# Kernel tuning notes

Measured on AMD Instinct MI355X. Metric: run time of the kernel, lower is better.

Reference implementation:

```python
import jax, jax.numpy as jnp
import numpy as np

N = 8192
D_MODEL = 256
D_K = 128
NUM_MOL = 512  # molecule_index values in [0, NUM_MOL); output rows = max(idx)+1, fixed here for jit


def setup_inputs() -> dict:
    key = jax.random.key(0)
    k1, k2, k3, k4, k5, k6, k7, k8 = jax.random.split(key, 8)
    fragments = jax.random.normal(k1, (N, D_MODEL), dtype=jnp.float32)
    molecule_index = jnp.sort(jax.random.randint(k2, (N,), 0, NUM_MOL, dtype=jnp.int64))
    s = 1.0 / np.sqrt(D_MODEL)
    Wq = jax.random.uniform(k3, (D_MODEL, D_K), jnp.float32, -s, s)
    bq = jax.random.uniform(k4, (D_K,), jnp.float32, -s, s)
    Wk = jax.random.uniform(k5, (D_MODEL, D_K), jnp.float32, -s, s)
    bk = jax.random.uniform(k6, (D_K,), jnp.float32, -s, s)
    Wv = jax.random.uniform(k7, (D_MODEL, D_K), jnp.float32, -s, s)
    bv = jax.random.uniform(k8, (D_K,), jnp.float32, -s, s)
    return {"fragments": fragments, "molecule_index": molecule_index,
            "Wq": Wq, "bq": bq, "Wk": Wk, "bk": bk, "Wv": Wv, "bv": bv}


def reference(fragments, molecule_index, Wq, bq, Wk, bk, Wv, bv):
    scale = jnp.asarray(np.sqrt(D_K), fragments.dtype)
    Q = fragments @ Wq + bq  # [N, d_k]
    K = fragments @ Wk + bk
    V = fragments @ Wv + bv
    scores = (Q / scale) @ K.T  # [N, N]
    same_mol = molecule_index[:, None] == molecule_index[None, :]
    scores = jnp.where(same_mol, scores, -jnp.inf)
    weights = jax.nn.softmax(scores, axis=-1)  # block-diagonal rows
    out = weights @ V  # [N, d_k]
    # scatter_add per-molecule pooling
    mol_emb = jax.ops.segment_sum(out, molecule_index, num_segments=NUM_MOL)
    return mol_emb
```

## Files before the change

### kernel.cpp

```cpp
#include <hip/hip_runtime.h>
#include <hip/hip_bf16.h>

#define D_MODEL 256
#define D_K 128
#define CH 48

typedef short bf16x8 __attribute__((ext_vector_type(8)));
typedef float f32x4 __attribute__((ext_vector_type(4)));

__device__ inline unsigned short f2bf(float x) {
    union { float f; unsigned u; } v; v.f = x;
    unsigned r = v.u + 0x7FFFu + ((v.u >> 16) & 1u);
    return (unsigned short)(r >> 16);
}
__device__ inline float bf2f(unsigned short h) {
    union { unsigned u; float f; } v; v.u = ((unsigned)h) << 16; return v.f;
}

#define AT_BYTE(r, c2) (((r) << 9) + ((((c2) << 1)) ^ (((r) & 7) << 4)))

__device__ __forceinline__ int wave_lb(const int* __restrict__ p, int stride, int n, int val, int guess) {
    const int lane = threadIdx.x & 63;
    int base = guess - 32;
    while (true) {
        int idx = base + lane;
        int v;
        if (idx < 0)        v = -2147483647 - 1;
        else if (idx >= n)  v = 2147483647;
        else                v = p[(size_t)idx * stride];
        unsigned long long ge = __ballot(v >= val);
        if (ge == 0ULL) { base += 64; continue; }
        int v0 = __shfl(v, 0);
        if (v0 >= val && base > 0) { base -= 63; continue; }
        return base + (__ffsll((unsigned long long)ge) - 1);
    }
}

__device__ __forceinline__ bf16x8 w_frag(const float* __restrict__ W, int cc, int k0, int g) {
    const float* p = W + (size_t)(k0 + g * 8) * D_K + cc;
    unsigned short t8[8];
    #pragma unroll
    for (int j = 0; j < 8; ++j) t8[j] = f2bf(p[(size_t)j * D_K]);
    return *(const bf16x8*)t8;
}

template<int NRT>
__device__ __forceinline__ void qkv_tiles(
    const unsigned char* lds,
    const float* __restrict__ Wq, const float* __restrict__ Wk, const float* __restrict__ Wv,
    int wave, int lr, int g, f32x4 (&acc)[6][NRT])
{
    #pragma unroll
    for (int cl = 0; cl < 6; ++cl) {
        const int ct = wave + cl * 4;
        const int which = ct >> 3, cc = (ct & 7) * 16 + lr;
        const float* W = which == 0 ? Wq : (which == 1 ? Wk : Wv);
        #pragma unroll
        for (int k0 = 0; k0 < 8; ++k0) {
            bf16x8 bf = w_frag(W, cc, k0 * 32, g);
            #pragma unroll
            for (int rt = 0; rt < NRT; ++rt) {
                bf16x8 af = *(const bf16x8*)(lds + AT_BYTE(rt * 16 + lr, k0 * 32 + g * 8));
                acc[cl][rt] = __builtin_amdgcn_mfma_f32_16x16x32_bf16(af, bf, acc[cl][rt], 0, 0, 0);
            }
        }
    }
}

template<int NRT>
__device__ __forceinline__ void fast_path(
    const float* __restrict__ A,
    const float* __restrict__ Wq, const float* __restrict__ bq,
    const float* __restrict__ Wk, const float* __restrict__ bk,
    const float* __restrict__ Wv, const float* __restrict__ bv,
    float* __restrict__ out, unsigned char* lds, int s, int m, int mol)
{
    unsigned short* Qb = (unsigned short*)(lds + 24576);
    unsigned short* Kb = (unsigned short*)(lds + 37632);
    unsigned short* Vb = (unsigned short*)(lds);
    unsigned short* S  = (unsigned short*)(lds + 50688);
    float* rinv = (float*)(lds + 55680);
    float* csum = (float*)(lds + 55872);
    float* emb  = (float*)(lds + 56064);

    const int tid = threadIdx.x;
    const int wave = tid >> 6, lane = tid & 63;
    const int lr = lane & 15, g = lane >> 4;

    #pragma unroll
    for (int it = 0; it < NRT * 4; ++it) {
        int eidx = tid * 4 + it * 1024;
        int r = eidx >> 8, c = eidx & 255;
        float4 a;
        if (r < m) a = *(const float4*)&A[(size_t)(s + r) * D_MODEL + c];
        else       a = make_float4(0.f, 0.f, 0.f, 0.f);
        unsigned short o[4] = {f2bf(a.x), f2bf(a.y), f2bf(a.z), f2bf(a.w)};
        *(unsigned long long*)(lds + AT_BYTE(r, c)) = *(const unsigned long long*)o;
    }
    __syncthreads();

    f32x4 acc[6][NRT];
    #pragma unroll
    for (int i = 0; i < 6; ++i)
        #pragma unroll
        for (int j = 0; j < NRT; ++j) acc[i][j] = {0.f, 0.f, 0.f, 0.f};
    qkv_tiles<NRT>(lds, Wq, Wk, Wv, wave, lr, g, acc);
    __syncthreads();

    const float qs = 0.08838834764831845f;
    #pragma unroll
    for (int cl = 0; cl < 6; ++cl) {
        int ct = wave + cl * 4;
        int which = ct >> 3;
        int col = (ct & 7) * 16 + lr;
        const float* bsrc = which == 0 ? bq : (which == 1 ? bk : bv);
        float bb = bsrc[col];
        float sc = which == 0 ? qs : 1.f;
        unsigned short* dst = which == 0 ? Qb : (which == 1 ? Kb : Vb);
        #pragma unroll
        for (int rt = 0; rt < NRT; ++rt) {
            int rbase = rt * 16 + g * 4;
            #pragma unroll
            for (int r = 0; r < 4; ++r)
                dst[(rbase + r) * 136 + col] = f2bf((acc[cl][rt][r] + bb) * sc);
        }
    }
    __syncthreads();

    for (int job = wave; job < NRT * NRT; job += 4) {
        int ti = job / NRT, tj = job % NRT;
        f32x4 sa = {0.f, 0.f, 0.f, 0.f};
        #pragma unroll
        for (int kk = 0; kk < 4; ++kk) {
            bf16x8 qf = *(const bf16x8*)&Qb[(ti * 16 + lr) * 136 + kk * 32 + g * 8];
            bf16x8 kf = *(const bf16x8*)&Kb[(tj * 16 + lr) * 136 + kk * 32 + g * 8];
            sa = __builtin_amdgcn_mfma_f32_16x16x32_bf16(qf, kf, sa, 0, 0, 0);
        }
        int jcol = tj * 16 + lr, ibase = ti * 16 + g * 4;
        #pragma unroll
        for (int r = 0; r < 4; ++r)
            S[(ibase + r) * 52 + jcol] = f2bf(sa[r]);
    }
    __syncthreads();

    {
        int row = tid >> 2, sub = tid & 3;
        if (row < m) {
            float mx = -3.4e38f;
            for (int j = sub; j < m; j += 4) mx = fmaxf(mx, bf2f(S[row * 52 + j]));
            mx = fmaxf(mx, __shfl_xor(mx, 1));
            mx = fmaxf(mx, __shfl_xor(mx, 2));
            float sum = 0.f;
            for (int j = sub; j < m; j += 4) {
                float ev = __expf(bf2f(S[row * 52 + j]) - mx);
                S[row * 52 + j] = f2bf(ev);
                sum += ev;
            }
            sum += __shfl_xor(sum, 1);
            sum += __shfl_xor(sum, 2);
            if (sub == 0) rinv[row] = 1.f / sum;
        }
    }
    __syncthreads();

    {
        int col = tid >> 2, sub = tid & 3;
        if (col < m) {
            float a = 0.f;
            for (int i = sub; i < m; i += 4) a += bf2f(S[i * 52 + col]) * rinv[i];
            a += __shfl_xor(a, 1);
            a += __shfl_xor(a, 2);
            if (sub == 0) csum[col] = a;
        }
    }
    __syncthreads();

    {
        int d = tid & 127, h = tid >> 7;
        float a = 0.f;
        for (int j = h; j < m; j += 2) a += csum[j] * bf2f(Vb[j * 136 + d]);
        emb[h * D_K + d] = a;
        __syncthreads();
        if (tid < D_K) out[(size_t)mol * D_K + tid] = emb[tid] + emb[D_K + tid];
    }
}

__global__ __launch_bounds__(256, 2) void fused_one(
    const float* __restrict__ A,
    const float* __restrict__ Wq, const float* __restrict__ bq,
    const float* __restrict__ Wk, const float* __restrict__ bk,
    const float* __restrict__ Wv, const float* __restrict__ bv,
    const int* __restrict__ midx,
    float* __restrict__ out,
    float* __restrict__ Qw, float* __restrict__ Kw, float* __restrict__ Vw,
    float* __restrict__ ML, int n, int nmol)
{
    __shared__ __align__(16) unsigned char lds[57088];
    int* se = (int*)(lds + 55680);

    const int tid = threadIdx.x, mol = blockIdx.x;
    const int wave = tid >> 6;

    const int stride = (midx[n - 1] == 0) ? 2 : 1;

    if (wave == 0) {
        int s_ = wave_lb(midx, stride, n, mol, (int)(((long long)mol * n) / nmol));
        if ((tid & 63) == 0) se[0] = s_;
    } else if (wave == 1) {
        int e_ = wave_lb(midx, stride, n, mol + 1, (int)(((long long)(mol + 1) * n) / nmol));
        if ((tid & 63) == 0) se[1] = e_;
    }
    __syncthreads();
    const int s = se[0], e = se[1];
    const int m = e - s;
    __syncthreads();

    if (m == 0) {
        if (tid < D_K) out[(size_t)mol * D_K + tid] = 0.f;
        return;
    }
    if (m <= 16) { fast_path<1>(A, Wq, bq, Wk, bk, Wv, bv, out, lds, s, m, mol); return; }
    if (m <= 32) { fast_path<2>(A, Wq, bq, Wk, bk, Wv, bv, out, lds, s, m, mol); return; }
    if (m <= 48) { fast_path<3>(A, Wq, bq, Wk, bk, Wv, bv, out, lds, s, m, mol); return; }

    const int lane = tid & 63;
    const int lr = lane & 15, g = lane >> 4;
    const float qs = 0.08838834764831845f;
    float* emb = (float*)(lds + 56064);

    for (int r0 = 0; r0 < m; r0 += CH) {
        #pragma unroll
        for (int it = 0; it < (CH * 256) / 1024; ++it) {
            int eidx = tid * 4 + it * 1024;
            int r = eidx >> 8, c = eidx & 255;
            float4 a;
            if (r0 + r < m) a = *(const float4*)&A[(size_t)(s + r0 + r) * D_MODEL + c];
            else            a = make_float4(0.f, 0.f, 0.f, 0.f);
            unsigned short o[4] = {f2bf(a.x), f2bf(a.y), f2bf(a.z), f2bf(a.w)};
            *(unsigned long long*)(lds + AT_BYTE(r, c)) = *(const unsigned long long*)o;
        }
        __syncthreads();

        f32x4 acc[6][3];
        #pragma unroll
        for (int i = 0; i < 6; ++i)
            #pragma unroll
            for (int j = 0; j < 3; ++j) acc[i][j] = {0.f, 0.f, 0.f, 0.f};
        qkv_tiles<3>(lds, Wq, Wk, Wv, wave, lr, g, acc);

        #pragma unroll
        for (int cl = 0; cl < 6; ++cl) {
            int ct = wave + cl * 4;
            int which = ct >> 3;
            int col = (ct & 7) * 16 + lr;
            const float* bsrc = which == 0 ? bq : (which == 1 ? bk : bv);
            float bb = bsrc[col];
            float sc = which == 0 ? qs : 1.f;
            float* dst = which == 0 ? Qw : (which == 1 ? Kw : Vw);
            #pragma unroll
            for (int rt = 0; rt < 3; ++rt) {
                int rbase = rt * 16 + g * 4;
                #pragma unroll
                for (int r = 0; r < 4; ++r) {
                    int lrow = rbase + r;
                    if (r0 + lrow < m)
                        dst[(size_t)(s + r0 + lrow) * D_K + col] = (acc[cl][rt][r] + bb) * sc;
                }
            }
        }
        __syncthreads();
    }

    if (tid < D_K) emb[tid] = 0.f;
    float* Mv = ML;
    float* Lv = ML + n;
    __threadfence();
    __syncthreads();

    for (int i = tid; i < m; i += 256) {
        const float4* q = (const float4*)(Qw + (size_t)(s + i) * D_K);
        float mx = -3.4e38f, sum = 0.f;
        for (int j = 0; j < m; ++j) {
            const float4* k = (const float4*)(Kw + (size_t)(s + j) * D_K);
            float sc = 0.f;
            #pragma unroll
            for (int t = 0; t < D_K / 4; ++t) {
                float4 a = q[t], b = k[t];
                sc += a.x * b.x + a.y * b.y + a.z * b.z + a.w * b.w;
            }
            if (sc > mx) { sum = sum * __expf(mx - sc) + 1.f; mx = sc; }
            else         { sum += __expf(sc - mx); }
        }
        Mv[s + i] = mx;
        Lv[s + i] = 1.f / sum;
    }
    __threadfence();
    __syncthreads();

    for (int j = tid; j < m; j += 256) {
        const float4* k = (const float4*)(Kw + (size_t)(s + j) * D_K);
        float cj = 0.f;
        for (int i = 0; i < m; ++i) {
            const float4* q = (const float4*)(Qw + (size_t)(s + i) * D_K);
            float sc = 0.f;
            #pragma unroll
            for (int t = 0; t < D_K / 4; ++t) {
                float4 a = q[t], b = k[t];
                sc += a.x * b.x + a.y * b.y + a.z * b.z + a.w * b.w;
            }
            cj += __expf(sc - Mv[s + i]) * Lv[s + i];
        }
        const float* v = Vw + (size_t)(s + j) * D_K;
        for (int d = 0; d < D_K; ++d) atomicAdd(&emb[d], cj * v[d]);
    }
    __syncthreads();
    if (tid < D_K) out[(size_t)mol * D_K + tid] = emb[tid];
}

extern "C" void kernel_launch(void* const* d_in, const int* in_sizes, int n_in,
                              void* d_out, int out_size, void* d_ws, size_t ws_size,
                              hipStream_t stream) {
    const float* frag = (const float*)d_in[0];
    const int*   midx = (const int*)d_in[1];
    const float* Wq = (const float*)d_in[2];
    const float* bq = (const float*)d_in[3];
    const float* Wk = (const float*)d_in[4];
    const float* bk = (const float*)d_in[5];
    const float* Wv = (const float*)d_in[6];
    const float* bv = (const float*)d_in[7];
    float* out = (float*)d_out;

    const int n = in_sizes[1];
    const int nmol = out_size / D_K;

    float* Qw = (float*)d_ws;
    float* Kw = Qw + (size_t)n * D_K;
    float* Vw = Kw + (size_t)n * D_K;
    float* ML = Vw + (size_t)n * D_K;

    fused_one<<<nmol, 256, 0, stream>>>(frag, Wq, bq, Wk, bk, Wv, bv, midx,
                                        out, Qw, Kw, Vw, ML, n, nmol);
}
```

Baseline: 19.80 us.

## Process molecule pairs per 512-thread block with masked joint attention tile

Each block now handles two consecutive molecules with 512 threads, packing both into one tile of up to 64 rows and masking cross-molecule scores to a large negative value so one softmax pass covers both. Weight fragments are now loaded by 8 waves with 3 column tiles each instead of 4 waves with 6, and a 64-row fast path is added. The aim is to halve block count, spread the W loads over more waves and fill MFMA tiles better for small molecules (about 16 rows on average). In exchange it uses more LDS per block, occupancy drops to one block per CU, and the masked tile computes wasted cross-molecule scores.

Measured after the change: 17.20 us. 13.2% less time.

```diff
diff --git a/kernel.cpp b/kernel.cpp
--- a/kernel.cpp
+++ b/kernel.cpp
@@ -4,6 +4,7 @@
 #define D_MODEL 256
 #define D_K 128
 #define CH 48
+#define NEG_BF16 ((unsigned short)0xFF7F)
 
 typedef short bf16x8 __attribute__((ext_vector_type(8)));
 typedef float f32x4 __attribute__((ext_vector_type(4)));
@@ -18,6 +19,12 @@
 }
 
 #define AT_BYTE(r, c2) (((r) << 9) + ((((c2) << 1)) ^ (((r) & 7) << 4)))
+#define QB_OFF 32768
+#define KB_OFF 50176
+#define S_OFF  67584
+#define RINV_OFF 76288
+#define CSUM_OFF 76544
+#define EMB_OFF  76800
 
 __device__ __forceinline__ int wave_lb(const int* __restrict__ p, int stride, int n, int val, int guess) {
     const int lane = threadIdx.x & 63;
@@ -48,11 +55,11 @@
 __device__ __forceinline__ void qkv_tiles(
     const unsigned char* lds,
     const float* __restrict__ Wq, const float* __restrict__ Wk, const float* __restrict__ Wv,
-    int wave, int lr, int g, f32x4 (&acc)[6][NRT])
+    int wave, int lr, int g, f32x4 (&acc)[3][NRT])
 {
     #pragma unroll
-    for (int cl = 0; cl < 6; ++cl) {
-        const int ct = wave + cl * 4;
+    for (int cl = 0; cl < 3; ++cl) {
+        const int ct = wave + cl * 8;
         const int which = ct >> 3, cc = (ct & 7) * 16 + lr;
         const float* W = which == 0 ? Wq : (which == 1 ? Wk : Wv);
         #pragma unroll
@@ -68,124 +75,252 @@
 }
 
 template<int NRT>
-__device__ __forceinline__ void fast_path(
+__device__ __forceinline__ void fast_pair(
+    const float* __restrict__ A,
+    const float* __restrict__ Wq, const float* __restrict__ bq,
+    const float* __restrict__ Wk, const float* __restrict__ bk,
+    const float* __restrict__ Wv, const float* __restrict__ bv,
+    float* __restrict__ out, unsigned char* lds,
+    int s, int mtot, int c1, int mol0, int mol1, bool w0, bool w1)
+{
+    unsigned short* Qb = (unsigned short*)(lds + QB_OFF);
+    unsigned short* Kb = (unsigned short*)(lds + KB_OFF);
+    unsigned short* Vb = (unsigned short*)(lds);
+    unsigned short* S  = (unsigned short*)(lds + S_OFF);
+    float* rinv = (float*)(lds + RINV_OFF);
+    float* csum = (float*)(lds + CSUM_OFF);
+    float* emb  = (float*)(lds + EMB_OFF);
+
+    const int tid = threadIdx.x;
+    const int wave = tid >> 6, lane = tid & 63;
+    const int lr = lane & 15, g = lane >> 4;
+
+    #pragma unroll
+    for (int it = 0; it < NRT * 2; ++it) {
+        int eidx = tid * 4 + it * 2048;
+        int r = eidx >> 8, c = eidx & 255;
+        float4 a;
+        if (r < mtot) a = *(const float4*)&A[(size_t)(s + r) * D_MODEL + c];
+        else          a = make_float4(0.f, 0.f, 0.f, 0.f);
+        unsigned short o[4] = {f2bf(a.x), f2bf(a.y), f2bf(a.z), f2bf(a.w)};
+        *(unsigned long long*)(lds + AT_BYTE(r, c)) = *(const unsigned long long*)o;
+    }
+    __syncthreads();
+
+    f32x4 acc[3][NRT];
+    #pragma unroll
+    for (int i = 0; i < 3; ++i)
+        #pragma unroll
+        for (int j = 0; j < NRT; ++j) acc[i][j] = {0.f, 0.f, 0.f, 0.f};
+    qkv_tiles<NRT>(lds, Wq, Wk, Wv, wave, lr, g, acc);
+    __syncthreads();
+
+    const float qs = 0.08838834764831845f;
+    #pragma unroll
+    for (int cl = 0; cl < 3; ++cl) {
+        int ct = wave + cl * 8;
+        int which = ct >> 3;
+        int col = (ct & 7) * 16 + lr;
+        const float* bsrc = which == 0 ? bq : (which == 1 ? bk : bv);
+        float bb = bsrc[col];
+        float sc = which == 0 ? qs : 1.f;
+        unsigned short* dst = which == 0 ? Qb : (which == 1 ? Kb : Vb);
+        #pragma unroll
+        for (int rt = 0; rt < NRT; ++rt) {
+            int rbase = rt * 16 + g * 4;
+            #pragma unroll
+            for (int r = 0; r < 4; ++r)
+                dst[(rbase + r) * 136 + col] = f2bf((acc[cl][rt][r] + bb) * sc);
+        }
+    }
+    __syncthreads();
+
+    for (int job = wave; job < NRT * NRT; job += 8) {
+        int ti = job / NRT, tj = job % NRT;
+        f32x4 sa = {0.f, 0.f, 0.f, 0.f};
+        #pragma unroll
+        for (int kk = 0; kk < 4; ++kk) {
+            bf16x8 qf = *(const bf16x8*)&Qb[(ti * 16 + lr) * 136 + kk * 32 + g * 8];
+            bf16x8 kf = *(const bf16x8*)&Kb[(tj * 16 + lr) * 136 + kk * 32 + g * 8];
+            sa = __builtin_amdgcn_mfma_f32_16x16x32_bf16(qf, kf, sa, 0, 0, 0);
+        }
+        int jcol = tj * 16 + lr, ibase = ti * 16 + g * 4;
+        bool jside = jcol < c1;
+        #pragma unroll
+        for (int r = 0; r < 4; ++r) {
+            bool same = ((ibase + r) < c1) == jside;
+            S[(ibase + r) * 68 + jcol] = same ? f2bf(sa[r]) : NEG_BF16;
+        }
+    }
+    __syncthreads();
+
+    {
+        int row = tid >> 2, sub = tid & 3;
+        if (row < mtot) {
+            float mx = -3.4e38f;
+            for (int j = sub; j < mtot; j += 4) mx = fmaxf(mx, bf2f(S[row * 68 + j]));
+            mx = fmaxf(mx, __shfl_xor(mx, 1));
+            mx = fmaxf(mx, __shfl_xor(mx, 2));
+            float sum = 0.f;
+            for (int j = sub; j < mtot; j += 4) {
+                float ev = __expf(bf2f(S[row * 68 + j]) - mx);
+                S[row * 68 + j] = f2bf(ev);
+                sum += ev;
+            }
+            sum += __shfl_xor(sum, 1);
+            sum += __shfl_xor(sum, 2);
+            if (sub == 0) rinv[row] = 1.f / sum;
+        }
+    }
+    __syncthreads();
+
+    {
+        int col = tid >> 2, sub = tid & 3;
+        if (col < mtot) {
+            float a = 0.f;
+            for (int i = sub; i < mtot; i += 4) a += bf2f(S[i * 68 + col]) * rinv[i];
+            a += __shfl_xor(a, 1);
+            a += __shfl_xor(a, 2);
+            if (sub == 0) csum[col] = a;
+        }
+    }
+    __syncthreads();
+
+    {
+        int d = tid & 127, h = tid >> 7;
+        float a = 0.f;
+        for (int j = h; j < c1; j += 4) a += csum[j] * bf2f(Vb[j * 136 + d]);
+        emb[h * D_K + d] = a;
+        __syncthreads();
+        if (w0 && tid < D_K)
+            out[(size_t)mol0 * D_K + tid] = emb[tid] + emb[D_K + tid] + emb[2 * D_K + tid] + emb[3 * D_K + tid];
+        __syncthreads();
+        a = 0.f;
+        for (int j = c1 + h; j < mtot; j += 4) a += csum[j] * bf2f(Vb[j * 136 + d]);
+        emb[h * D_K + d] = a;
+        __syncthreads();
+        if (w1 && tid < D_K)
+            out[(size_t)mol1 * D_K + tid] = emb[tid] + emb[D_K + tid] + emb[2 * D_K + tid] + emb[3 * D_K + tid];
+    }
+}
+
+__device__ __forceinline__ void run_single(
     const float* __restrict__ A,
     const float* __restrict__ Wq, const float* __restrict__ bq,
     const float* __restrict__ Wk, const float* __restrict__ bk,
     const float* __restrict__ Wv, const float* __restrict__ bv,
     float* __restrict__ out, unsigned char* lds, int s, int m, int mol)
 {
-    unsigned short* Qb = (unsigned short*)(lds + 24576);
-    unsigned short* Kb = (unsigned short*)(lds + 37632);
-    unsigned short* Vb = (unsigned short*)(lds);
-    unsigned short* S  = (unsigned short*)(lds + 50688);
-    float* rinv = (float*)(lds + 55680);
-    float* csum = (float*)(lds + 55872);
-    float* emb  = (float*)(lds + 56064);
-
+    if (m <= 16)      fast_pair<1>(A, Wq, bq, Wk, bk, Wv, bv, out, lds, s, m, m, mol, mol, true, false);
+    else if (m <= 32) fast_pair<2>(A, Wq, bq, Wk, bk, Wv, bv, out, lds, s, m, m, mol, mol, true, false);
+    else if (m <= 48) fast_pair<3>(A, Wq, bq, Wk, bk, Wv, bv, out, lds, s, m, m, mol, mol, true, false);
+    else              fast_pair<4>(A, Wq, bq, Wk, bk, Wv, bv, out, lds, s, m, m, mol, mol, true, false);
+}
+
+__device__ void slow_stream(
+    const float* __restrict__ A,
+    const float* __restrict__ Wq, const float* __restrict__ bq,
+    const float* __restrict__ Wk, const float* __restrict__ bk,
+    const float* __restrict__ Wv, const float* __restrict__ bv,
+    float* __restrict__ out, unsigned char* lds,
+    float* __restrict__ Qw, float* __restrict__ Kw, float* __restrict__ Vw,
+    float* __restrict__ ML, int s, int m, int mol, int n)
+{
     const int tid = threadIdx.x;
     const int wave = tid >> 6, lane = tid & 63;
     const int lr = lane & 15, g = lane >> 4;
-
-    #pragma unroll
-    for (int it = 0; it < NRT * 4; ++it) {
-        int eidx = tid * 4 + it * 1024;
-        int r = eidx >> 8, c = eidx & 255;
-        float4 a;
-        if (r < m) a = *(const float4*)&A[(size_t)(s + r) * D_MODEL + c];
-        else       a = make_float4(0.f, 0.f, 0.f, 0.f);
-        unsigned short o[4] = {f2bf(a.x), f2bf(a.y), f2bf(a.z), f2bf(a.w)};
-        *(unsigned long long*)(lds + AT_BYTE(r, c)) = *(const unsigned long long*)o;
-    }
-    __syncthreads();
-
-    f32x4 acc[6][NRT];
-    #pragma unroll
-    for (int i = 0; i < 6; ++i)
-        #pragma unroll
-        for (int j = 0; j < NRT; ++j) acc[i][j] = {0.f, 0.f, 0.f, 0.f};
-    qkv_tiles<NRT>(lds, Wq, Wk, Wv, wave, lr, g, acc);
-    __syncthreads();
-
     const float qs = 0.08838834764831845f;
-    #pragma unroll
-    for (int cl = 0; cl < 6; ++cl) {
-        int ct = wave + cl * 4;
-        int which = ct >> 3;
-        int col = (ct & 7) * 16 + lr;
-        const float* bsrc = which == 0 ? bq : (which == 1 ? bk : bv);
-        float bb = bsrc[col];
-        float sc = which == 0 ? qs : 1.f;
-        unsigned short* dst = which == 0 ? Qb : (which == 1 ? Kb : Vb);
-        #pragma unroll
-        for (int rt = 0; rt < NRT; ++rt) {
-            int rbase = rt * 16 + g * 4;
-            #pragma unroll
-            for (int r = 0; r < 4; ++r)
-                dst[(rbase + r) * 136 + col] = f2bf((acc[cl][rt][r] + bb) * sc);
-        }
-    }
-    __syncthreads();
-
-    for (int job = wave; job < NRT * NRT; job += 4) {
-        int ti = job / NRT, tj = job % NRT;
-        f32x4 sa = {0.f, 0.f, 0.f, 0.f};
-        #pragma unroll
-        for (int kk = 0; kk < 4; ++kk) {
-            bf16x8 qf = *(const bf16x8*)&Qb[(ti * 16 + lr) * 136 + kk * 32 + g * 8];
-            bf16x8 kf = *(const bf16x8*)&Kb[(tj * 16 + lr) * 136 + kk * 32 + g * 8];
-            sa = __builtin_amdgcn_mfma_f32_16x16x32_bf16(qf, kf, sa, 0, 0, 0);
-        }
-        int jcol = tj * 16 + lr, ibase = ti * 16 + g * 4;
-        #pragma unroll
-        for (int r = 0; r < 4; ++r)
-            S[(ibase + r) * 52 + jcol] = f2bf(sa[r]);
-    }
-    __syncthreads();
-
-    {
-        int row = tid >> 2, sub = tid & 3;
-        if (row < m) {
-            float mx = -3.4e38f;
-            for (int j = sub; j < m; j += 4) mx = fmaxf(mx, bf2f(S[row * 52 + j]));
-            mx = fmaxf(mx, __shfl_xor(mx, 1));
-            mx = fmaxf(mx, __shfl_xor(mx, 2));
-            float sum = 0.f;
-            for (int j = sub; j < m; j += 4) {
-                float ev = __expf(bf2f(S[row * 52 + j]) - mx);
-                S[row * 52 + j] = f2bf(ev);
-                sum += ev;
+    float* emb = (float*)(lds + EMB_OFF);
+
+    for (int r0 = 0; r0 < m; r0 += CH) {
+        for (int it = 0; it < (CH * 256) / 2048; ++it) {
+            int eidx = tid * 4 + it * 2048;
+            int r = eidx >> 8, c = eidx & 255;
+            float4 a;
+            if (r0 + r < m) a = *(const float4*)&A[(size_t)(s + r0 + r) * D_MODEL + c];
+            else            a = make_float4(0.f, 0.f, 0.f, 0.f);
+            unsigned short o[4] = {f2bf(a.x), f2bf(a.y), f2bf(a.z), f2bf(a.w)};
+            *(unsigned long long*)(lds + AT_BYTE(r, c)) = *(const unsigned long long*)o;
+        }
+        __syncthreads();
+
+        f32x4 acc[3][3];
+        #pragma unroll
+        for (int i = 0; i < 3; ++i)
+            #pragma unroll
+            for (int j = 0; j < 3; ++j) acc[i][j] = {0.f, 0.f, 0.f, 0.f};
+        qkv_tiles<3>(lds, Wq, Wk, Wv, wave, lr, g, acc);
+
+        #pragma unroll
+        for (int cl = 0; cl < 3; ++cl) {
+            int ct = wave + cl * 8;
+            int which = ct >> 3;
+            int col = (ct & 7) * 16 + lr;
+            const float* bsrc = which == 0 ? bq : (which == 1 ? bk : bv);
+            float bb = bsrc[col];
+            float sc = which == 0 ? qs : 1.f;
+            float* dst = which == 0 ? Qw : (which == 1 ? Kw : Vw);
+            #pragma unroll
+            for (int rt = 0; rt < 3; ++rt) {
+                int rbase = rt * 16 + g * 4;
+                #pragma unroll
+                for (int r = 0; r < 4; ++r) {
+                    int lrow = rbase + r;
+                    if (r0 + lrow < m)
+                        dst[(size_t)(s + r0 + lrow) * D_K + col] = (acc[cl][rt][r] + bb) * sc;
+                }
             }
-            sum += __shfl_xor(sum, 1);
-            sum += __shfl_xor(sum, 2);
-            if (sub == 0) rinv[row] = 1.f / sum;
-        }
-    }
-    __syncthreads();
-
-    {
-        int col = tid >> 2, sub = tid & 3;
-        if (col < m) {
-            float a = 0.f;
-            for (int i = sub; i < m; i += 4) a += bf2f(S[i * 52 + col]) * rinv[i];
-            a += __shfl_xor(a, 1);
-            a += __shfl_xor(a, 2);
-            if (sub == 0) csum[col] = a;
-        }
-    }
-    __syncthreads();
-
-    {
-        int d = tid & 127, h = tid >> 7;
-        float a = 0.f;
-        for (int j = h; j < m; j += 2) a += csum[j] * bf2f(Vb[j * 136 + d]);
-        emb[h * D_K + d] = a;
+        }
         __syncthreads();
-        if (tid < D_K) out[(size_t)mol * D_K + tid] = emb[tid] + emb[D_K + tid];
-    }
-}
-
-__global__ __launch_bounds__(256, 2) void fused_one(
+    }
+
+    if (tid < D_K) emb[tid] = 0.f;
+    float* Mv = ML;
+    float* Lv = ML + n;
+    __threadfence();
+    __syncthreads();
+
+    for (int i = tid; i < m; i += 512) {
+        const float4* q = (const float4*)(Qw + (size_t)(s + i) * D_K);
+        float mx = -3.4e38f, sum = 0.f;
+        for (int j = 0; j < m; ++j) {
+            const float4* k = (const float4*)(Kw + (size_t)(s + j) * D_K);
+            float sc = 0.f;
+            #pragma unroll
+            for (int t = 0; t < D_K / 4; ++t) {
+                float4 a = q[t], b = k[t];
+                sc += a.x * b.x + a.y * b.y + a.z * b.z + a.w * b.w;
+            }
+            if (sc > mx) { sum = sum * __expf(mx - sc) + 1.f; mx = sc; }
+            else         { sum += __expf(sc - mx); }
+        }
+        Mv[s + i] = mx;
+        Lv[s + i] = 1.f / sum;
+    }
+    __threadfence();
+    __syncthreads();
+
+    for (int j = tid; j < m; j += 512) {
+        const float4* k = (const float4*)(Kw + (size_t)(s + j) * D_K);
+        float cj = 0.f;
+        for (int i = 0; i < m; ++i) {
+            const float4* q = (const float4*)(Qw + (size_t)(s + i) * D_K);
+            float sc = 0.f;
+            #pragma unroll
+            for (int t = 0; t < D_K / 4; ++t) {
+                float4 a = q[t], b = k[t];
+                sc += a.x * b.x + a.y * b.y + a.z * b.z + a.w * b.w;
+            }
+            cj += __expf(sc - Mv[s + i]) * Lv[s + i];
+        }
+        const float* v = Vw + (size_t)(s + j) * D_K;
+        for (int d = 0; d < D_K; ++d) atomicAdd(&emb[d], cj * v[d]);
+    }
+    __syncthreads();
+    if (tid < D_K) out[(size_t)mol * D_K + tid] = emb[tid];
+}
+
+__global__ __launch_bounds__(512, 1) void fused_pair(
     const float* __restrict__ A,
     const float* __restrict__ Wq, const float* __restrict__ bq,
     const float* __restrict__ Wk, const float* __restrict__ bk,
@@ -195,126 +330,52 @@
     float* __restrict__ Qw, float* __restrict__ Kw, float* __restrict__ Vw,
     float* __restrict__ ML, int n, int nmol)
 {
-    __shared__ __align__(16) unsigned char lds[57088];
-    int* se = (int*)(lds + 55680);
-
-    const int tid = threadIdx.x, mol = blockIdx.x;
+    __shared__ __align__(16) unsigned char lds[78848];
+    int* se = (int*)(lds + RINV_OFF);
+
+    const int tid = threadIdx.x;
     const int wave = tid >> 6;
+    const int mol0 = blockIdx.x * 2;
+    const int mol1 = mol0 + 1;
+    const bool haveM1 = mol1 < nmol;
 
     const int stride = (midx[n - 1] == 0) ? 2 : 1;
 
-    if (wave == 0) {
-        int s_ = wave_lb(midx, stride, n, mol, (int)(((long long)mol * n) / nmol));
-        if ((tid & 63) == 0) se[0] = s_;
-    } else if (wave == 1) {
-        int e_ = wave_lb(midx, stride, n, mol + 1, (int)(((long long)(mol + 1) * n) / nmol));
-        if ((tid & 63) == 0) se[1] = e_;
-    }
-    __syncthreads();
-    const int s = se[0], e = se[1];
-    const int m = e - s;
-    __syncthreads();
-
-    if (m == 0) {
-        if (tid < D_K) out[(size_t)mol * D_K + tid] = 0.f;
+    if (wave < 3) {
+        int val = mol0 + wave;
+        if (val > nmol) val = nmol;
+        int r = wave_lb(midx, stride, n, val, (int)(((long long)val * n) / nmol));
+        if ((tid & 63) == 0) se[wave] = r;
+    }
+    __syncthreads();
+    const int s0 = se[0], s1 = se[1], e = se[2];
+    __syncthreads();
+
+    const int m0 = s1 - s0, m1 = e - s1, mtot = e - s0;
+    const int c1 = m0;
+
+    if (mtot == 0) {
+        if (tid < D_K) out[(size_t)mol0 * D_K + tid] = 0.f;
+        else if (haveM1 && tid < 2 * D_K) out[(size_t)mol1 * D_K + (tid - D_K)] = 0.f;
         return;
     }
-    if (m <= 16) { fast_path<1>(A, Wq, bq, Wk, bk, Wv, bv, out, lds, s, m, mol); return; }
-    if (m <= 32) { fast_path<2>(A, Wq, bq, Wk, bk, Wv, bv, out, lds, s, m, mol); return; }
-    if (m <= 48) { fast_path<3>(A, Wq, bq, Wk, bk, Wv, bv, out, lds, s, m, mol); return; }
-
-    const int lane = tid & 63;
-    const int lr = lane & 15, g = lane >> 4;
-    const float qs = 0.08838834764831845f;
-    float* emb = (float*)(lds + 56064);
-
-    for (int r0 = 0; r0 < m; r0 += CH) {
-        #pragma unroll
-        for (int it = 0; it < (CH * 256) / 1024; ++it) {
-            int eidx = tid * 4 + it * 1024;
-            int r = eidx >> 8, c = eidx & 255;
-            float4 a;
-            if (r0 + r < m) a = *(const float4*)&A[(size_t)(s + r0 + r) * D_MODEL + c];
-            else            a = make_float4(0.f, 0.f, 0.f, 0.f);
-            unsigned short o[4] = {f2bf(a.x), f2bf(a.y), f2bf(a.z), f2bf(a.w)};
-            *(unsigned long long*)(lds + AT_BYTE(r, c)) = *(const unsigned long long*)o;
-        }
-        __syncthreads();
-
-        f32x4 acc[6][3];
-        #pragma unroll
-        for (int i = 0; i < 6; ++i)
-            #pragma unroll
-            for (int j = 0; j < 3; ++j) acc[i][j] = {0.f, 0.f, 0.f, 0.f};
-        qkv_tiles<3>(lds, Wq, Wk, Wv, wave, lr, g, acc);
-
-        #pragma unroll
-        for (int cl = 0; cl < 6; ++cl) {
-            int ct = wave + cl * 4;
-            int which = ct >> 3;
-            int col = (ct & 7) * 16 + lr;
-            const float* bsrc = which == 0 ? bq : (which == 1 ? bk : bv);
-            float bb = bsrc[col];
-            float sc = which == 0 ? qs : 1.f;
-            float* dst = which == 0 ? Qw : (which == 1 ? Kw : Vw);
-            #pragma unroll
-            for (int rt = 0; rt < 3; ++rt) {
-                int rbase = rt * 16 + g * 4;
-                #pragma unroll
-                for (int r = 0; r < 4; ++r) {
-                    int lrow = rbase + r;
-                    if (r0 + lrow < m)
-                        dst[(size_t)(s + r0 + lrow) * D_K + col] = (acc[cl][rt][r] + bb) * sc;
-                }
-            }
-        }
-        __syncthreads();
-    }
-
-    if (tid < D_K) emb[tid] = 0.f;
-    float* Mv = ML;
-    float* Lv = ML + n;
-    __threadfence();
-    __syncthreads();
-
-    for (int i = tid; i < m; i += 256) {
-        const float4* q = (const float4*)(Qw + (size_t)(s + i) * D_K);
-        float mx = -3.4e38f, sum = 0.f;
-        for (int j = 0; j < m; ++j) {
-            const float4* k = (const float4*)(Kw + (size_t)(s + j) * D_K);
-            float sc = 0.f;
-            #pragma unroll
-            for (int t = 0; t < D_K / 4; ++t) {
-                float4 a = q[t], b = k[t];
-                sc += a.x * b.x + a.y * b.y + a.z * b.z + a.w * b.w;
-            }
-            if (sc > mx) { sum = sum * __expf(mx - sc) + 1.f; mx = sc; }
-            else         { sum += __expf(sc - mx); }
-        }
-        Mv[s + i] = mx;
-        Lv[s + i] = 1.f / sum;
-    }
-    __threadfence();
-    __syncthreads();
-
-    for (int j = tid; j < m; j += 256) {
-        const float4* k = (const float4*)(Kw + (size_t)(s + j) * D_K);
-        float cj = 0.f;
-        for (int i = 0; i < m; ++i) {
-            const float4* q = (const float4*)(Qw + (size_t)(s + i) * D_K);
-            float sc = 0.f;
-            #pragma unroll
-            for (int t = 0; t < D_K / 4; ++t) {
-                float4 a = q[t], b = k[t];
-                sc += a.x * b.x + a.y * b.y + a.z * b.z + a.w * b.w;
-            }
-            cj += __expf(sc - Mv[s + i]) * Lv[s + i];
-        }
-        const float* v = Vw + (size_t)(s + j) * D_K;
-        for (int d = 0; d < D_K; ++d) atomicAdd(&emb[d], cj * v[d]);
-    }
-    __syncthreads();
-    if (tid < D_K) out[(size_t)mol * D_K + tid] = emb[tid];
+
+    if (mtot <= 64) {
+        if (mtot <= 16)      fast_pair<1>(A, Wq, bq, Wk, bk, Wv, bv, out, lds, s0, mtot, c1, mol0, mol1, true, haveM1);
+        else if (mtot <= 32) fast_pair<2>(A, Wq, bq, Wk, bk, Wv, bv, out, lds, s0, mtot, c1, mol0, mol1, true, haveM1);
+        else if (mtot <= 48) fast_pair<3>(A, Wq, bq, Wk, bk, Wv, bv, out, lds, s0, mtot, c1, mol0, mol1, true, haveM1);
+        else                 fast_pair<4>(A, Wq, bq, Wk, bk, Wv, bv, out, lds, s0, mtot, c1, mol0, mol1, true, haveM1);
+        return;
+    }
+
+    if (m0 <= 64) run_single(A, Wq, bq, Wk, bk, Wv, bv, out, lds, s0, m0, mol0);
+    else          slow_stream(A, Wq, bq, Wk, bk, Wv, bv, out, lds, Qw, Kw, Vw, ML, s0, m0, mol0, n);
+    __syncthreads();
+    if (haveM1) {
+        if (m1 == 0) { if (tid < D_K) out[(size_t)mol1 * D_K + tid] = 0.f; return; }
+        if (m1 <= 64) run_single(A, Wq, bq, Wk, bk, Wv, bv, out, lds, s1, m1, mol1);
+        else          slow_stream(A, Wq, bq, Wk, bk, Wv, bv, out, lds, Qw, Kw, Vw, ML, s1, m1, mol1, n);
+    }
 }
 
 extern "C" void kernel_launch(void* const* d_in, const int* in_sizes, int n_in,
@@ -338,6 +399,7 @@
     float* Vw = Kw + (size_t)n * D_K;
     float* ML = Vw + (size_t)n * D_K;
 
-    fused_one<<<nmol, 256, 0, stream>>>(frag, Wq, bq, Wk, bk, Wv, bv, midx,
-                                        out, Qw, Kw, Vw, ML, n, nmol);
-}
+    const int nblocks = (nmol + 1) / 2;
+    fused_pair<<<nblocks, 512, 0, stream>>>(frag, Wq, bq, Wk, bk, Wv, bv, midx,
+                                            out, Qw, Kw, Vw, ML, n, nmol);
+}
```
